# Optimization experiments

Measured on AMD Instinct MI355X. Metric: run time of the kernel, lower is better.

The kernel has to match this reference:

```python
import jax, jax.numpy as jnp
import numpy as np
from jax import lax

H = 65  # hidden size

def lstm_layer(x, w_ih, w_hh, b_ih, b_hh):
    # x: [B, T, in]; w_ih: [4H, in]; w_hh: [4H, H]; PyTorch gate order i,f,g,o
    B = x.shape[0]
    # precompute input contribution for all timesteps: [T, B, 4H]
    pre = jnp.einsum('bti,gi->tbg', x, w_ih) + (b_ih + b_hh)
    wh = w_hh.T  # [H, 4H]

    def step(carry, pre_t):
        h, c = carry
        gates = pre_t + h @ wh
        i, f, g, o = jnp.split(gates, 4, axis=-1)
        i = jax.nn.sigmoid(i)
        f = jax.nn.sigmoid(f)
        g = jnp.tanh(g)
        o = jax.nn.sigmoid(o)
        c = f * c + i * g
        h = o * jnp.tanh(c)
        return (h, c), h

    init = (jnp.zeros((B, H), x.dtype), jnp.zeros((B, H), x.dtype))
    _, hs = lax.scan(step, init, pre)  # hs: [T, B, H]
    return jnp.transpose(hs, (1, 0, 2))  # [B, T, H]


def setup_inputs() -> dict:
    key = jax.random.key(0)
    ks = jax.random.split(key, 11)
    B, T = 512, 1024
    s = 1.0 / np.sqrt(H)
    d = {
        'x': jax.random.normal(ks[0], (B, T, H), jnp.float32),
        'w_ih0': jax.random.normal(ks[1], (4 * H, H), jnp.float32) * s,
        'w_hh0': jax.random.normal(ks[2], (4 * H, H), jnp.float32) * s,
        'b_ih0': jax.random.normal(ks[3], (4 * H,), jnp.float32) * s,
        'b_hh0': jax.random.normal(ks[4], (4 * H,), jnp.float32) * s,
        'w_ih1': jax.random.normal(ks[5], (4 * H, H), jnp.float32) * s,
        'w_hh1': jax.random.normal(ks[6], (4 * H, H), jnp.float32) * s,
        'b_ih1': jax.random.normal(ks[7], (4 * H,), jnp.float32) * s,
        'b_hh1': jax.random.normal(ks[8], (4 * H,), jnp.float32) * s,
        'w_lin': jax.random.normal(ks[9], (1, H), jnp.float32) * s,
        'b_lin': jax.random.normal(ks[10], (1,), jnp.float32) * s,
    }
    return d


def reference(x, w_ih0, w_hh0, b_ih0, b_hh0, w_ih1, w_hh1, b_ih1, b_hh1, w_lin, b_lin):
    h1 = lstm_layer(x, w_ih0, w_hh0, b_ih0, b_hh0)   # [B, T, H]
    h2 = lstm_layer(h1, w_ih1, w_hh1, b_ih1, b_hh1)  # [B, T, H]
    last = h2[:, -1, :]                               # [B, H]
    return last @ w_lin.T + b_lin                     # [B, 1]
```

## Files before the change

### kernel.cpp

```cpp
#include <hip/hip_runtime.h>

#define H 65
#define T_STEPS 1024

typedef _Float16 half_t;
typedef _Float16 half2_t __attribute__((ext_vector_type(2)));

static __device__ __forceinline__ float dot2(half2_t a, half2_t b, float c) {
#if __has_builtin(__builtin_amdgcn_fdot2)
  return __builtin_amdgcn_fdot2(a, b, c, false);
#else
  float d;
  asm("v_dot2_f32_f16 %0, %1, %2, %3" : "=v"(d) : "v"(a), "v"(b), "v"(c));
  return d;
#endif
}

template <int CTRL>
static __device__ __forceinline__ float qperm(float v) {
  int r = __builtin_amdgcn_update_dpp(0, __builtin_bit_cast(int, v), CTRL, 0xF, 0xF, true);
  return __builtin_bit_cast(float, r);
}

template <int PAT>
static __device__ __forceinline__ float swz(float v) {
  int r = __builtin_amdgcn_ds_swizzle(__builtin_bit_cast(int, v), PAT);
  return __builtin_bit_cast(float, r);
}

#define LOG2E 1.44269504089f
static __device__ __forceinline__ float fast_sigm(float v) {
  float e = __builtin_amdgcn_exp2f(-LOG2E * v);
  return __builtin_amdgcn_rcpf(1.f + e);
}

static __device__ __forceinline__ float pick(int idx, float a, float b, float c, float d) {
  float lo = (idx & 1) ? b : a;
  float hi = (idx & 1) ? d : c;
  return (idx & 2) ? hi : lo;
}

__global__ __launch_bounds__(512, 2) void lstm_fused(
    const float* __restrict__ x,
    const float* __restrict__ wih0, const float* __restrict__ whh0,
    const float* __restrict__ bih0, const float* __restrict__ bhh0,
    const float* __restrict__ wih1, const float* __restrict__ whh1,
    const float* __restrict__ bih1, const float* __restrict__ bhh1,
    const float* __restrict__ wlin, const float* __restrict__ blin,
    float* __restrict__ out)
{
  __shared__ __align__(16) half_t xh[2][2][2][144];
  __shared__ float h1f[2][H];

  const int tid = threadIdx.x;

  const int quad = tid >> 2;
  const int l  = (quad >= 65) ? 1 : 0;
  const int j  = quad - 65 * l;
  const int kh = (tid >> 1) & 1;
  const int g0 = tid & 1;
  const bool gz = (g0 == 0);
  const float mreg = gz ? 2.f : 1.f;
  const float msub = mreg - 1.f;

  half2_t w[2][33];
  float hb[2];
  {
    const float* wi = l ? wih1 : wih0;
    const float* wh = l ? whh1 : whh0;
    const float* bi = l ? bih1 : bih0;
    const float* bh = l ? bhh1 : bhh0;
#pragma unroll
    for (int cc = 0; cc < 2; ++cc) {
      const int row = (g0 + 2 * cc) * H + j;
      hb[cc] = 0.5f * (bi[row] + bh[row]);
      const float* src = (kh ? wh : wi) + row * H;
#pragma unroll
      for (int pp = 0; pp < 33; ++pp) {
        float e0 = src[2 * pp];
        float e1 = (2 * pp + 1 < H) ? src[2 * pp + 1] : 0.f;
        half2_t v = {(half_t)e0, (half_t)e1};
        w[cc][pp] = v;
      }
    }
  }

  const bool isW7 = (tid >= 448);
  const int  w7   = tid - 448;
  const int  ec   = w7 >> 3;
  const int  ck   = w7 & 7;
  const int  side = ck >> 2;
  const int  sck  = ck & 3;
  const int  ecoff = side * 144 + 36 * sck;
  half2_t ecw[9];
  float ecbias = 0.f;
  float cecA = 0.f, cecB = 0.f;
  if (isW7) {
    const int gec = ec & 3;
    const int jec = 63 + (ec >> 2);
    const int row = gec * H + jec;
    const float* src = (side ? whh1 : wih1) + row * H;
#pragma unroll
    for (int i = 0; i < 9; ++i) {
      int es = 9 * sck + i;
      float e0 = (es < 33) ? src[2 * es] : 0.f;
      float e1 = (es < 33 && 2 * es + 1 < H) ? src[2 * es + 1] : 0.f;
      half2_t v = {(half_t)e0, (half_t)e1};
      ecw[i] = v;
    }
    if (ck == 0) ecbias = bih1[row] + bhh1[row];
  } else {
#pragma unroll
    for (int i = 0; i < 9; ++i) {
      half2_t z = {(half_t)0.f, (half_t)0.f};
      ecw[i] = z;
    }
  }

  const bool isW6 = (tid >= 384) && (tid < 448);
  const int  u    = tid - 384;

  for (int i = tid; i < 2 * 2 * 2 * 144; i += 512) ((half_t*)xh)[i] = (half_t)0.f;
  __syncthreads();

  const float* xrowA = x + (size_t)(2 * blockIdx.x)     * (size_t)(T_STEPS * H);
  const float* xrowB = x + (size_t)(2 * blockIdx.x + 1) * (size_t)(T_STEPS * H);
  float nA = 0.f, nA64 = 0.f, nB = 0.f, nB64 = 0.f;
  if (isW6) {
    xh[0][0][0][u] = (half_t)xrowA[u];
    xh[1][0][0][u] = (half_t)xrowB[u];
    if (u == 0) {
      xh[0][0][0][64] = (half_t)xrowA[64];
      xh[1][0][0][64] = (half_t)xrowB[64];
    }
    nA = xrowA[H + u];
    nB = xrowB[H + u];
    if (u == 0) { nA64 = xrowA[H + 64]; nB64 = xrowB[H + 64]; }
  }
  __syncthreads();

  float cstA = 0.f, cstB = 0.f;

  for (int s = 0; s <= T_STEPS; ++s) {
    const int p = s & 1;

    float fA = 0.f, fA64 = 0.f, fB = 0.f, fB64 = 0.f;
    if (isW6 && (s + 2 < T_STEPS)) {
      const float* xrA = xrowA + (size_t)(s + 2) * H;
      const float* xrB = xrowB + (size_t)(s + 2) * H;
      fA = xrA[u];
      fB = xrB[u];
      if (u == 0) { fA64 = xrA[64]; fB64 = xrB[64]; }
    }

    const bool act = l ? (s >= 1) : (s < T_STEPS);
    if (act) {
      const half_t* xbA = &xh[0][l][p][0] + 72 * kh;
      const half_t* xbB = &xh[1][l][p][0] + 72 * kh;
      float a0A = hb[0], a1A = hb[1];
      float a0B = hb[0], a1B = hb[1];
#pragma unroll
      for (int c = 0; c < 8; ++c) {
        uint4 qA = ((const uint4*)xbA)[c];
        uint4 qB = ((const uint4*)xbB)[c];
        half2_t xA0 = __builtin_bit_cast(half2_t, qA.x);
        half2_t xA1 = __builtin_bit_cast(half2_t, qA.y);
        half2_t xA2 = __builtin_bit_cast(half2_t, qA.z);
        half2_t xA3 = __builtin_bit_cast(half2_t, qA.w);
        half2_t xB0 = __builtin_bit_cast(half2_t, qB.x);
        half2_t xB1 = __builtin_bit_cast(half2_t, qB.y);
        half2_t xB2 = __builtin_bit_cast(half2_t, qB.z);
        half2_t xB3 = __builtin_bit_cast(half2_t, qB.w);
        a0A = dot2(xA0, w[0][4 * c + 0], a0A);
        a0B = dot2(xB0, w[0][4 * c + 0], a0B);
        a1A = dot2(xA0, w[1][4 * c + 0], a1A);
        a1B = dot2(xB0, w[1][4 * c + 0], a1B);
        a0A = dot2(xA1, w[0][4 * c + 1], a0A);
        a0B = dot2(xB1, w[0][4 * c + 1], a0B);
        a1A = dot2(xA1, w[1][4 * c + 1], a1A);
        a1B = dot2(xB1, w[1][4 * c + 1], a1B);
        a0A = dot2(xA2, w[0][4 * c + 2], a0A);
        a0B = dot2(xB2, w[0][4 * c + 2], a0B);
        a1A = dot2(xA2, w[1][4 * c + 2], a1A);
        a1B = dot2(xB2, w[1][4 * c + 2], a1B);
        a0A = dot2(xA3, w[0][4 * c + 3], a0A);
        a0B = dot2(xB3, w[0][4 * c + 3], a0B);
        a1A = dot2(xA3, w[1][4 * c + 3], a1A);
        a1B = dot2(xB3, w[1][4 * c + 3], a1B);
      }
      {
        half2_t xtA = *(const half2_t*)(xbA + 64);
        half2_t xtB = *(const half2_t*)(xbB + 64);
        a0A = dot2(xtA, w[0][32], a0A);
        a0B = dot2(xtB, w[0][32], a0B);
        a1A = dot2(xtA, w[1][32], a1A);
        a1B = dot2(xtB, w[1][32], a1B);
      }
      a0A += qperm<0x4E>(a0A);
      a1A += qperm<0x4E>(a1A);
      a0B += qperm<0x4E>(a0B);
      a1B += qperm<0x4E>(a1B);
      float e0A = fast_sigm(a0A);
      float e1A = mreg * fast_sigm(mreg * a1A) - msub;
      float e0B = fast_sigm(a0B);
      float e1B = mreg * fast_sigm(mreg * a1B) - msub;
      float p0A = qperm<0xB1>(e0A);
      float p1A = qperm<0xB1>(e1A);
      float p0B = qperm<0xB1>(e0B);
      float p1B = qperm<0xB1>(e1B);
      float ivA = gz ? e0A : p0A, fvA = gz ? p0A : e0A;
      float gvA = gz ? e1A : p1A, ovA = gz ? p1A : e1A;
      float ivB = gz ? e0B : p0B, fvB = gz ? p0B : e0B;
      float gvB = gz ? e1B : p1B, ovB = gz ? p1B : e1B;
      cstA = fvA * cstA + ivA * gvA;
      cstB = fvB * cstB + ivB * gvB;
      float thA = 2.f * fast_sigm(2.f * cstA) - 1.f;
      float thB = 2.f * fast_sigm(2.f * cstB) - 1.f;
      float hvA = ovA * thA;
      float hvB = ovB * thB;
      if ((tid & 3) == 0) {
        half_t hA = (half_t)hvA;
        half_t hB = (half_t)hvB;
        if (l == 0) {
          xh[0][0][p ^ 1][72 + j] = hA;
          xh[0][1][p ^ 1][j]      = hA;
          xh[1][0][p ^ 1][72 + j] = hB;
          xh[1][1][p ^ 1][j]      = hB;
        } else {
          xh[0][1][p ^ 1][72 + j] = hA;
          xh[1][1][p ^ 1][72 + j] = hB;
          if (s == T_STEPS) { h1f[0][j] = hvA; h1f[1][j] = hvB; }
        }
      }
    }

    if (isW7 && s >= 1) {
      const char* xbA1 = (const char*)&xh[0][1][p][0];
      const char* xbB1 = (const char*)&xh[1][1][p][0];
      float aecA = ecbias, aecB = ecbias;
#pragma unroll
      for (int i = 0; i < 9; ++i) {
        unsigned qA = *(const unsigned*)(xbA1 + ecoff + 4 * i);
        unsigned qB = *(const unsigned*)(xbB1 + ecoff + 4 * i);
        aecA = dot2(__builtin_bit_cast(half2_t, qA), ecw[i], aecA);
        aecB = dot2(__builtin_bit_cast(half2_t, qB), ecw[i], aecB);
      }
      aecA += swz<0x041F>(aecA);
      aecB += swz<0x041F>(aecB);
      aecA += swz<0x081F>(aecA);
      aecB += swz<0x081F>(aecB);
      aecA += swz<0x101F>(aecA);
      aecB += swz<0x101F>(aecB);
      const int gec = ec & 3;
      float me = (gec == 2) ? 2.f : 1.f;
      float AA = me * fast_sigm(me * aecA) - (me - 1.f);
      float AB = me * fast_sigm(me * aecB) - (me - 1.f);
      float BvA = swz<0x201F>(AA);
      float BvB = swz<0x201F>(AB);
      float CvA = swz<0x401F>(AA);
      float CvB = swz<0x401F>(AB);
      float DvA = swz<0x401F>(BvA);
      float DvB = swz<0x401F>(BvB);
      float ivA2 = pick(gec ^ 0, AA, BvA, CvA, DvA);
      float fvA2 = pick(gec ^ 1, AA, BvA, CvA, DvA);
      float gvA2 = pick(gec ^ 2, AA, BvA, CvA, DvA);
      float ovA2 = pick(gec ^ 3, AA, BvA, CvA, DvA);
      float ivB2 = pick(gec ^ 0, AB, BvB, CvB, DvB);
      float fvB2 = pick(gec ^ 1, AB, BvB, CvB, DvB);
      float gvB2 = pick(gec ^ 2, AB, BvB, CvB, DvB);
      float ovB2 = pick(gec ^ 3, AB, BvB, CvB, DvB);
      cecA = fvA2 * cecA + ivA2 * gvA2;
      cecB = fvB2 * cecB + ivB2 * gvB2;
      float hecA = ovA2 * (2.f * fast_sigm(2.f * cecA) - 1.f);
      float hecB = ovB2 * (2.f * fast_sigm(2.f * cecB) - 1.f);
      if (ck == 0 && (ec & 3) == 0) {
        const int jec = 63 + (ec >> 2);
        xh[0][1][p ^ 1][72 + jec] = (half_t)hecA;
        xh[1][1][p ^ 1][72 + jec] = (half_t)hecB;
        if (s == T_STEPS) { h1f[0][jec] = hecA; h1f[1][jec] = hecB; }
      }
    }

    if (isW6 && (s + 1 < T_STEPS)) {
      half_t* dA = &xh[0][0][p ^ 1][0];
      half_t* dB = &xh[1][0][p ^ 1][0];
      dA[u] = (half_t)nA;
      dB[u] = (half_t)nB;
      if (u == 0) { dA[64] = (half_t)nA64; dB[64] = (half_t)nB64; }
      nA = fA; nA64 = fA64; nB = fB; nB64 = fB64;
    }
    __syncthreads();
  }

  if (tid == 0) {
    float acc0 = blin[0], acc1 = blin[0];
    for (int jj = 0; jj < H; ++jj) {
      acc0 += h1f[0][jj] * wlin[jj];
      acc1 += h1f[1][jj] * wlin[jj];
    }
    out[2 * blockIdx.x]     = acc0;
    out[2 * blockIdx.x + 1] = acc1;
  }
}

extern "C" void kernel_launch(void* const* d_in, const int* in_sizes, int n_in,
                              void* d_out, int out_size, void* d_ws, size_t ws_size,
                              hipStream_t stream) {
  const float* x    = (const float*)d_in[0];
  const float* wih0 = (const float*)d_in[1];
  const float* whh0 = (const float*)d_in[2];
  const float* bih0 = (const float*)d_in[3];
  const float* bhh0 = (const float*)d_in[4];
  const float* wih1 = (const float*)d_in[5];
  const float* whh1 = (const float*)d_in[6];
  const float* bih1 = (const float*)d_in[7];
  const float* bhh1 = (const float*)d_in[8];
  const float* wlin = (const float*)d_in[9];
  const float* blin = (const float*)d_in[10];
  float* out = (float*)d_out;

  lstm_fused<<<256, 512, 0, stream>>>(x, wih0, whh0, bih0, bhh0,
                                      wih1, whh1, bih1, bhh1, wlin, blin, out);
}
```

Baseline: 1.520 ms.

## Add 1024-thread LSTM kernel splitting reduction over 8 lanes with interleaved batch layout

Adds a new 1024-thread kernel in which each hidden unit is handled by 8 lanes instead of 4. Each lane does a quarter of the combined input+hidden dot product, and the two batch rows are interleaved in shared memory so a single 16-byte load feeds both. This shortens each thread's serial dot chain per timestep, at the cost of more threads, an extra cross-lane reduction, and higher register pressure. The original 512-thread kernel is kept as a fallback, chosen at runtime when the new kernel spills to scratch, and its edge-unit work is split across two waves by batch row. The fallback's stager moves to wave 0.

```diff
diff --git a/kernel.cpp b/kernel.cpp
--- a/kernel.cpp
+++ b/kernel.cpp
@@ -40,7 +40,266 @@
   return (idx & 2) ? hi : lo;
 }
 
-__global__ __launch_bounds__(512, 2) void lstm_fused(
+__global__
+__attribute__((amdgpu_flat_work_group_size(1024, 1024)))
+void lstm_fused_a(
+    const float* __restrict__ x,
+    const float* __restrict__ wih0, const float* __restrict__ whh0,
+    const float* __restrict__ bih0, const float* __restrict__ bhh0,
+    const float* __restrict__ wih1, const float* __restrict__ whh1,
+    const float* __restrict__ bih1, const float* __restrict__ bhh1,
+    const float* __restrict__ wlin, const float* __restrict__ blin,
+    float* __restrict__ out)
+{
+  __shared__ __align__(16) unsigned char xh2[2][2][576];
+  __shared__ float h1f[2][H];
+
+  const int tid = threadIdx.x;
+
+  const int oct = tid >> 3;
+  const int l  = (oct >= 65) ? 1 : 0;
+  const int j  = oct - 65 * l;
+  const int kq = (tid >> 1) & 3;
+  const int g0 = tid & 1;
+  const bool gz = (g0 == 0);
+  const float mreg = gz ? 2.f : 1.f;
+  const float msub = mreg - 1.f;
+
+  half2_t w[2][18];
+  float hb[2];
+  {
+    const float* wi = l ? wih1 : wih0;
+    const float* wh = l ? whh1 : whh0;
+    const float* bi = l ? bih1 : bih0;
+    const float* bh = l ? bhh1 : bhh0;
+#pragma unroll
+    for (int cc = 0; cc < 2; ++cc) {
+      const int row = (g0 + 2 * cc) * H + j;
+      hb[cc] = 0.25f * (bi[row] + bh[row]);
+      const float* wiR = wi + row * H;
+      const float* whR = wh + row * H;
+#pragma unroll
+      for (int pp = 0; pp < 18; ++pp) {
+        const int bp0 = 36 * kq + 2 * pp;
+        const int bp1 = bp0 + 1;
+        float e0 = (bp0 < 65) ? wiR[bp0] : ((bp0 >= 72 && bp0 < 137) ? whR[bp0 - 72] : 0.f);
+        float e1 = (bp1 < 65) ? wiR[bp1] : ((bp1 >= 72 && bp1 < 137) ? whR[bp1 - 72] : 0.f);
+        half2_t v = {(half_t)e0, (half_t)e1};
+        w[cc][pp] = v;
+      }
+    }
+  }
+
+  const bool isW7 = (tid >= 960);
+  const int  w7   = tid - 960;
+  const int  ec   = w7 >> 3;
+  const int  ck   = w7 & 7;
+  const int  side = ck >> 2;
+  const int  sck  = ck & 3;
+  const int  ecoff2 = 2 * (side * 144 + 36 * sck);
+  half2_t ecw[9];
+  float ecbias = 0.f;
+  float cecA = 0.f, cecB = 0.f;
+  if (isW7) {
+    const int gec = ec & 3;
+    const int jec = 63 + (ec >> 2);
+    const int row = gec * H + jec;
+    const float* src = (side ? whh1 : wih1) + row * H;
+#pragma unroll
+    for (int i = 0; i < 9; ++i) {
+      int es = 9 * sck + i;
+      float e0 = (es < 33) ? src[2 * es] : 0.f;
+      float e1 = (es < 33 && 2 * es + 1 < H) ? src[2 * es + 1] : 0.f;
+      half2_t v = {(half_t)e0, (half_t)e1};
+      ecw[i] = v;
+    }
+    if (ck == 0) ecbias = bih1[row] + bhh1[row];
+  } else {
+#pragma unroll
+    for (int i = 0; i < 9; ++i) {
+      half2_t z = {(half_t)0.f, (half_t)0.f};
+      ecw[i] = z;
+    }
+  }
+
+  const bool isW6 = (tid >= 896) && (tid < 960);
+  const int  u    = tid - 896;
+  const int  uoffA = 8 * (u >> 1) + 2 * (u & 1);
+
+  for (int i = tid; i < 2 * 2 * 576; i += 1024) ((unsigned char*)xh2)[i] = 0;
+  __syncthreads();
+
+  const float* xrowA = x + (size_t)(2 * blockIdx.x)     * (size_t)(T_STEPS * H);
+  const float* xrowB = x + (size_t)(2 * blockIdx.x + 1) * (size_t)(T_STEPS * H);
+  float nA = 0.f, nA64 = 0.f, nB = 0.f, nB64 = 0.f;
+  if (isW6) {
+    unsigned char* d0 = &xh2[0][0][0];
+    *(half_t*)(d0 + uoffA)     = (half_t)xrowA[u];
+    *(half_t*)(d0 + uoffA + 4) = (half_t)xrowB[u];
+    if (u == 0) {
+      *(half_t*)(d0 + 256)     = (half_t)xrowA[64];
+      *(half_t*)(d0 + 260)     = (half_t)xrowB[64];
+    }
+    nA = xrowA[H + u];
+    nB = xrowB[H + u];
+    if (u == 0) { nA64 = xrowA[H + 64]; nB64 = xrowB[H + 64]; }
+  }
+  __syncthreads();
+
+  float cstA = 0.f, cstB = 0.f;
+
+  for (int s = 0; s <= T_STEPS; ++s) {
+    const int p = s & 1;
+
+    float fA = 0.f, fA64 = 0.f, fB = 0.f, fB64 = 0.f;
+    if (isW6 && (s + 2 < T_STEPS)) {
+      const float* xrA = xrowA + (size_t)(s + 2) * H;
+      const float* xrB = xrowB + (size_t)(s + 2) * H;
+      fA = xrA[u];
+      fB = xrB[u];
+      if (u == 0) { fA64 = xrA[64]; fB64 = xrB[64]; }
+    }
+
+    const bool act = l ? (s >= 1) : (s < T_STEPS);
+    if (act) {
+      const unsigned char* xb = &xh2[l][p][0] + 144 * kq;
+      float a0A = hb[0], a1A = hb[1];
+      float a0B = hb[0], a1B = hb[1];
+#pragma unroll
+      for (int c = 0; c < 9; ++c) {
+        uint4 qv = ((const uint4*)xb)[c];
+        half2_t pA0 = __builtin_bit_cast(half2_t, qv.x);
+        half2_t pB0 = __builtin_bit_cast(half2_t, qv.y);
+        half2_t pA1 = __builtin_bit_cast(half2_t, qv.z);
+        half2_t pB1 = __builtin_bit_cast(half2_t, qv.w);
+        a0A = dot2(pA0, w[0][2 * c + 0], a0A);
+        a0B = dot2(pB0, w[0][2 * c + 0], a0B);
+        a1A = dot2(pA0, w[1][2 * c + 0], a1A);
+        a1B = dot2(pB0, w[1][2 * c + 0], a1B);
+        a0A = dot2(pA1, w[0][2 * c + 1], a0A);
+        a0B = dot2(pB1, w[0][2 * c + 1], a0B);
+        a1A = dot2(pA1, w[1][2 * c + 1], a1A);
+        a1B = dot2(pB1, w[1][2 * c + 1], a1B);
+      }
+      a0A += qperm<0x4E>(a0A);
+      a1A += qperm<0x4E>(a1A);
+      a0B += qperm<0x4E>(a0B);
+      a1B += qperm<0x4E>(a1B);
+      a0A += swz<0x101F>(a0A);
+      a1A += swz<0x101F>(a1A);
+      a0B += swz<0x101F>(a0B);
+      a1B += swz<0x101F>(a1B);
+      float e0A = fast_sigm(a0A);
+      float e1A = mreg * fast_sigm(mreg * a1A) - msub;
+      float e0B = fast_sigm(a0B);
+      float e1B = mreg * fast_sigm(mreg * a1B) - msub;
+      float p0A = qperm<0xB1>(e0A);
+      float p1A = qperm<0xB1>(e1A);
+      float p0B = qperm<0xB1>(e0B);
+      float p1B = qperm<0xB1>(e1B);
+      float ivA = gz ? e0A : p0A, fvA = gz ? p0A : e0A;
+      float gvA = gz ? e1A : p1A, ovA = gz ? p1A : e1A;
+      float ivB = gz ? e0B : p0B, fvB = gz ? p0B : e0B;
+      float gvB = gz ? e1B : p1B, ovB = gz ? p1B : e1B;
+      cstA = fvA * cstA + ivA * gvA;
+      cstB = fvB * cstB + ivB * gvB;
+      float thA = 2.f * fast_sigm(2.f * cstA) - 1.f;
+      float thB = 2.f * fast_sigm(2.f * cstB) - 1.f;
+      float hvA = ovA * thA;
+      float hvB = ovB * thB;
+      if ((tid & 7) == 0) {
+        half_t hA = (half_t)hvA;
+        half_t hB = (half_t)hvB;
+        const int hoff = 288 + 8 * (j >> 1) + 2 * (j & 1);
+        const int xoff = 8 * (j >> 1) + 2 * (j & 1);
+        if (l == 0) {
+          unsigned char* d00 = &xh2[0][p ^ 1][0];
+          unsigned char* d10 = &xh2[1][p ^ 1][0];
+          *(half_t*)(d00 + hoff)     = hA;
+          *(half_t*)(d00 + hoff + 4) = hB;
+          *(half_t*)(d10 + xoff)     = hA;
+          *(half_t*)(d10 + xoff + 4) = hB;
+        } else {
+          unsigned char* d11 = &xh2[1][p ^ 1][0];
+          *(half_t*)(d11 + hoff)     = hA;
+          *(half_t*)(d11 + hoff + 4) = hB;
+          if (s == T_STEPS) { h1f[0][j] = hvA; h1f[1][j] = hvB; }
+        }
+      }
+    }
+
+    if (isW7 && s >= 1) {
+      const unsigned char* xb1 = &xh2[1][p][0];
+      float aecA = ecbias, aecB = ecbias;
+#pragma unroll
+      for (int i = 0; i < 9; ++i) {
+        uint2 qv = *(const uint2*)(xb1 + ecoff2 + 8 * i);
+        aecA = dot2(__builtin_bit_cast(half2_t, qv.x), ecw[i], aecA);
+        aecB = dot2(__builtin_bit_cast(half2_t, qv.y), ecw[i], aecB);
+      }
+      aecA += swz<0x041F>(aecA);
+      aecB += swz<0x041F>(aecB);
+      aecA += swz<0x081F>(aecA);
+      aecB += swz<0x081F>(aecB);
+      aecA += swz<0x101F>(aecA);
+      aecB += swz<0x101F>(aecB);
+      const int gec = ec & 3;
+      float me = (gec == 2) ? 2.f : 1.f;
+      float AA = me * fast_sigm(me * aecA) - (me - 1.f);
+      float AB = me * fast_sigm(me * aecB) - (me - 1.f);
+      float BvA = swz<0x201F>(AA);
+      float BvB = swz<0x201F>(AB);
+      float CvA = swz<0x401F>(AA);
+      float CvB = swz<0x401F>(AB);
+      float DvA = swz<0x401F>(BvA);
+      float DvB = swz<0x401F>(BvB);
+      float ivA2 = pick(gec ^ 0, AA, BvA, CvA, DvA);
+      float fvA2 = pick(gec ^ 1, AA, BvA, CvA, DvA);
+      float gvA2 = pick(gec ^ 2, AA, BvA, CvA, DvA);
+      float ovA2 = pick(gec ^ 3, AA, BvA, CvA, DvA);
+      float ivB2 = pick(gec ^ 0, AB, BvB, CvB, DvB);
+      float fvB2 = pick(gec ^ 1, AB, BvB, CvB, DvB);
+      float gvB2 = pick(gec ^ 2, AB, BvB, CvB, DvB);
+      float ovB2 = pick(gec ^ 3, AB, BvB, CvB, DvB);
+      cecA = fvA2 * cecA + ivA2 * gvA2;
+      cecB = fvB2 * cecB + ivB2 * gvB2;
+      float hecA = ovA2 * (2.f * fast_sigm(2.f * cecA) - 1.f);
+      float hecB = ovB2 * (2.f * fast_sigm(2.f * cecB) - 1.f);
+      if (ck == 0 && (ec & 3) == 0) {
+        const int jec = 63 + (ec >> 2);
+        const int hoff = 288 + 8 * (jec >> 1) + 2 * (jec & 1);
+        unsigned char* d11 = &xh2[1][p ^ 1][0];
+        *(half_t*)(d11 + hoff)     = (half_t)hecA;
+        *(half_t*)(d11 + hoff + 4) = (half_t)hecB;
+        if (s == T_STEPS) { h1f[0][jec] = hecA; h1f[1][jec] = hecB; }
+      }
+    }
+
+    if (isW6 && (s + 1 < T_STEPS)) {
+      unsigned char* d0 = &xh2[0][p ^ 1][0];
+      *(half_t*)(d0 + uoffA)     = (half_t)nA;
+      *(half_t*)(d0 + uoffA + 4) = (half_t)nB;
+      if (u == 0) {
+        *(half_t*)(d0 + 256) = (half_t)nA64;
+        *(half_t*)(d0 + 260) = (half_t)nB64;
+      }
+      nA = fA; nA64 = fA64; nB = fB; nB64 = fB64;
+    }
+    __syncthreads();
+  }
+
+  if (tid == 0) {
+    float acc0 = blin[0], acc1 = blin[0];
+    for (int jj = 0; jj < H; ++jj) {
+      acc0 += h1f[0][jj] * wlin[jj];
+      acc1 += h1f[1][jj] * wlin[jj];
+    }
+    out[2 * blockIdx.x]     = acc0;
+    out[2 * blockIdx.x + 1] = acc1;
+  }
+}
+
+__global__ __launch_bounds__(512, 1) void lstm_fused_512(
     const float* __restrict__ x,
     const float* __restrict__ wih0, const float* __restrict__ whh0,
     const float* __restrict__ bih0, const float* __restrict__ bhh0,
@@ -85,17 +344,18 @@
     }
   }
 
-  const bool isW7 = (tid >= 448);
-  const int  w7   = tid - 448;
-  const int  ec   = w7 >> 3;
-  const int  ck   = w7 & 7;
+  const bool isEC = (tid >= 384);
+  const int  e6   = tid & 63;
+  const int  ecR  = (tid >> 6) & 1;
+  const int  ec   = e6 >> 3;
+  const int  ck   = e6 & 7;
   const int  side = ck >> 2;
   const int  sck  = ck & 3;
   const int  ecoff = side * 144 + 36 * sck;
   half2_t ecw[9];
   float ecbias = 0.f;
-  float cecA = 0.f, cecB = 0.f;
-  if (isW7) {
+  float cec = 0.f;
+  if (isEC) {
     const int gec = ec & 3;
     const int jec = 63 + (ec >> 2);
     const int row = gec * H + jec;
@@ -117,8 +377,8 @@
     }
   }
 
-  const bool isW6 = (tid >= 384) && (tid < 448);
-  const int  u    = tid - 384;
+  const bool isST = (tid < 64);
+  const int  u    = tid;
 
   for (int i = tid; i < 2 * 2 * 2 * 144; i += 512) ((half_t*)xh)[i] = (half_t)0.f;
   __syncthreads();
@@ -126,7 +386,7 @@
   const float* xrowA = x + (size_t)(2 * blockIdx.x)     * (size_t)(T_STEPS * H);
   const float* xrowB = x + (size_t)(2 * blockIdx.x + 1) * (size_t)(T_STEPS * H);
   float nA = 0.f, nA64 = 0.f, nB = 0.f, nB64 = 0.f;
-  if (isW6) {
+  if (isST) {
     xh[0][0][0][u] = (half_t)xrowA[u];
     xh[1][0][0][u] = (half_t)xrowB[u];
     if (u == 0) {
@@ -145,7 +405,7 @@
     const int p = s & 1;
 
     float fA = 0.f, fA64 = 0.f, fB = 0.f, fB64 = 0.f;
-    if (isW6 && (s + 2 < T_STEPS)) {
+    if (isST && (s + 2 < T_STEPS)) {
       const float* xrA = xrowA + (size_t)(s + 2) * H;
       const float* xrB = xrowB + (size_t)(s + 2) * H;
       fA = xrA[u];
@@ -234,54 +494,37 @@
       }
     }
 
-    if (isW7 && s >= 1) {
-      const char* xbA1 = (const char*)&xh[0][1][p][0];
-      const char* xbB1 = (const char*)&xh[1][1][p][0];
-      float aecA = ecbias, aecB = ecbias;
+    if (isEC && s >= 1) {
+      const char* xb1 = (const char*)&xh[ecR][1][p][0];
+      float aec = ecbias;
 #pragma unroll
       for (int i = 0; i < 9; ++i) {
-        unsigned qA = *(const unsigned*)(xbA1 + ecoff + 4 * i);
-        unsigned qB = *(const unsigned*)(xbB1 + ecoff + 4 * i);
-        aecA = dot2(__builtin_bit_cast(half2_t, qA), ecw[i], aecA);
-        aecB = dot2(__builtin_bit_cast(half2_t, qB), ecw[i], aecB);
-      }
-      aecA += swz<0x041F>(aecA);
-      aecB += swz<0x041F>(aecB);
-      aecA += swz<0x081F>(aecA);
-      aecB += swz<0x081F>(aecB);
-      aecA += swz<0x101F>(aecA);
-      aecB += swz<0x101F>(aecB);
+        unsigned qv = *(const unsigned*)(xb1 + ecoff + 4 * i);
+        aec = dot2(__builtin_bit_cast(half2_t, qv), ecw[i], aec);
+      }
+      aec += swz<0x041F>(aec);
+      aec += swz<0x081F>(aec);
+      aec += swz<0x101F>(aec);
       const int gec = ec & 3;
       float me = (gec == 2) ? 2.f : 1.f;
-      float AA = me * fast_sigm(me * aecA) - (me - 1.f);
-      float AB = me * fast_sigm(me * aecB) - (me - 1.f);
-      float BvA = swz<0x201F>(AA);
-      float BvB = swz<0x201F>(AB);
-      float CvA = swz<0x401F>(AA);
-      float CvB = swz<0x401F>(AB);
-      float DvA = swz<0x401F>(BvA);
-      float DvB = swz<0x401F>(BvB);
-      float ivA2 = pick(gec ^ 0, AA, BvA, CvA, DvA);
-      float fvA2 = pick(gec ^ 1, AA, BvA, CvA, DvA);
-      float gvA2 = pick(gec ^ 2, AA, BvA, CvA, DvA);
-      float ovA2 = pick(gec ^ 3, AA, BvA, CvA, DvA);
-      float ivB2 = pick(gec ^ 0, AB, BvB, CvB, DvB);
-      float fvB2 = pick(gec ^ 1, AB, BvB, CvB, DvB);
-      float gvB2 = pick(gec ^ 2, AB, BvB, CvB, DvB);
-      float ovB2 = pick(gec ^ 3, AB, BvB, CvB, DvB);
-      cecA = fvA2 * cecA + ivA2 * gvA2;
-      cecB = fvB2 * cecB + ivB2 * gvB2;
-      float hecA = ovA2 * (2.f * fast_sigm(2.f * cecA) - 1.f);
-      float hecB = ovB2 * (2.f * fast_sigm(2.f * cecB) - 1.f);
+      float A  = me * fast_sigm(me * aec) - (me - 1.f);
+      float Bv = swz<0x201F>(A);
+      float Cv = swz<0x401F>(A);
+      float Dv = swz<0x401F>(Bv);
+      float iv2 = pick(gec ^ 0, A, Bv, Cv, Dv);
+      float fv2 = pick(gec ^ 1, A, Bv, Cv, Dv);
+      float gv2 = pick(gec ^ 2, A, Bv, Cv, Dv);
+      float ov2 = pick(gec ^ 3, A, Bv, Cv, Dv);
+      cec = fv2 * cec + iv2 * gv2;
+      float hec = ov2 * (2.f * fast_sigm(2.f * cec) - 1.f);
       if (ck == 0 && (ec & 3) == 0) {
         const int jec = 63 + (ec >> 2);
-        xh[0][1][p ^ 1][72 + jec] = (half_t)hecA;
-        xh[1][1][p ^ 1][72 + jec] = (half_t)hecB;
-        if (s == T_STEPS) { h1f[0][jec] = hecA; h1f[1][jec] = hecB; }
-      }
-    }
-
-    if (isW6 && (s + 1 < T_STEPS)) {
+        xh[ecR][1][p ^ 1][72 + jec] = (half_t)hec;
+        if (s == T_STEPS) h1f[ecR][jec] = hec;
+      }
+    }
+
+    if (isST && (s + 1 < T_STEPS)) {
       half_t* dA = &xh[0][0][p ^ 1][0];
       half_t* dB = &xh[1][0][p ^ 1][0];
       dA[u] = (half_t)nA;
@@ -319,6 +562,22 @@
   const float* blin = (const float*)d_in[10];
   float* out = (float*)d_out;
 
-  lstm_fused<<<256, 512, 0, stream>>>(x, wih0, whh0, bih0, bhh0,
-                                      wih1, whh1, bih1, bhh1, wlin, blin, out);
-}
+  static int useA = -1;
+  if (useA < 0) {
+    hipFuncAttributes a{};
+    if (hipFuncGetAttributes(&a, reinterpret_cast<const void*>(&lstm_fused_a)) == hipSuccess &&
+        a.localSizeBytes <= 40) {
+      useA = 1;
+    } else {
+      useA = 0;
+    }
+  }
+
+  if (useA) {
+    lstm_fused_a<<<256, 1024, 0, stream>>>(x, wih0, whh0, bih0, bhh0,
+                                           wih1, whh1, bih1, bhh1, wlin, blin, out);
+  } else {
+    lstm_fused_512<<<256, 512, 0, stream>>>(x, wih0, whh0, bih0, bhh0,
+                                            wih1, whh1, bih1, bhh1, wlin, blin, out);
+  }
+}
```

Result: slower. 1.826 ms (+20.2%).
